# Kernel optimization log

Measured on AMD Instinct MI355X. Metric: run time of the kernel, lower is better.

Reference implementation:

```python
import jax, jax.numpy as jnp
import numpy as np

GAMMA = 1.0

def _rbf_mean(a, b, gamma):
    # mean of exp(-gamma * ||a_i - b_j||^2) over the full [Na, Nb] kernel matrix
    aa = jnp.sum(a * a, axis=1, keepdims=True)          # [Na, 1]
    bb = jnp.sum(b * b, axis=1, keepdims=True)          # [Nb, 1]
    dist = aa + bb.T - 2.0 * (a @ b.T)                  # [Na, Nb]
    return jnp.mean(jnp.exp(-gamma * dist))

def setup_inputs() -> dict:
    key = jax.random.key(0)
    kx, ky = jax.random.split(key)
    N, D = 8192, 128
    x = jax.random.normal(kx, (N, D), dtype=jnp.float32)
    y = jax.random.normal(ky, (N, D), dtype=jnp.float32)
    return {"x": x, "y": y}

def reference(x, y):
    mmd = (_rbf_mean(x, x, GAMMA)
           + _rbf_mean(y, y, GAMMA)
           - 2.0 * _rbf_mean(x, y, GAMMA))
    return mmd
```

## Files before the change

kernel.cpp:

```cpp
#include <hip/hip_runtime.h>


#define N_PTS 8192
#define DCOLS 128
#define TILE 128
#define TJ 64
#define NSELF 2080
#define NJOBS 8256
#define NBLOCKS 768
#define LOG2E 1.4426950408889634f
#define THRESH -40.0f
#define QS 24.0f
#define INV_S2 (1.0f / (QS * QS))

typedef __attribute__((ext_vector_type(4))) int int4v;
typedef unsigned int u32;
typedef unsigned short u16;
typedef unsigned char u8;

#if __has_builtin(__builtin_amdgcn_exp2f)
#define EXP2(x) __builtin_amdgcn_exp2f(x)
#else
#define EXP2(x) exp2f(x)
#endif

__device__ __forceinline__ int vmax(int a, int b) { return a > b ? a : b; }

__device__ __forceinline__ void gl_lds16(const u8* g, u8* l) {
  __builtin_amdgcn_global_load_lds(
      (const __attribute__((address_space(1))) u32*)g,
      (__attribute__((address_space(3))) u32*)l, 16, 0, 0);
}

__global__ void prep_kernel(const float* __restrict__ x, const float* __restrict__ y,
                            u32* __restrict__ xb, u32* __restrict__ yb,
                            float* __restrict__ da, float* __restrict__ db,
                            u32* __restrict__ Sz) {
  if (blockIdx.x == 0 && threadIdx.x < 4) Sz[threadIdx.x] = 0;
  int gt = blockIdx.x * 256 + threadIdx.x;
  int r = gt >> 5;
  int l31 = threadIdx.x & 31;
  const float* src;
  u32* dst;
  float* dn;
  int rr = r;
  if (r < N_PTS) { src = x; dst = xb; dn = da; }
  else           { src = y; dst = yb; dn = db; rr = r - N_PTS; }
  float4 v = ((const float4*)(src + (size_t)rr * 128))[l31];
  int q0 = (int)rintf(fminf(fmaxf(v.x * QS, -127.f), 127.f));
  int q1 = (int)rintf(fminf(fmaxf(v.y * QS, -127.f), 127.f));
  int q2 = (int)rintf(fminf(fmaxf(v.z * QS, -127.f), 127.f));
  int q3 = (int)rintf(fminf(fmaxf(v.w * QS, -127.f), 127.f));
  dst[(size_t)rr * 32 + l31] = (u32)(q0 & 0xff) | ((u32)(q1 & 0xff) << 8) |
                               ((u32)(q2 & 0xff) << 16) | ((u32)(q3 & 0xff) << 24);
  int p = q0 * q0 + q1 * q1 + q2 * q2 + q3 * q3;
#pragma unroll
  for (int off = 16; off; off >>= 1) p += __shfl_xor(p, off, 64);
  if (l31 == 0) dn[rr] = -LOG2E * INV_S2 * (float)p;
}

struct Job { int pair, rr, cc; };

__device__ __forceinline__ Job decode_job(int t) {
  Job jb;
  if (t < 2 * NSELF) {
    jb.pair = (t < NSELF) ? 0 : 1;
    int tt = t - jb.pair * NSELF;
    int r = 0;
    while (tt >= TJ - r) { tt -= TJ - r; r++; }
    jb.rr = r; jb.cc = r + tt;
  } else {
    int q = t - 2 * NSELF;
    jb.pair = 2; jb.rr = q >> 6; jb.cc = q & 63;
  }
  return jb;
}

__device__ __forceinline__ Job next_job(Job c) {
  Job n = c;
  if (c.pair == 2) {
    if (c.cc == 63) { n.rr++; n.cc = 0; } else n.cc++;
  } else {
    if (c.cc == 63) {
      if (c.rr == 63) { n.pair++; n.rr = 0; n.cc = 0; }
      else { n.rr++; n.cc = n.rr; }
    } else n.cc++;
  }
  return n;
}

__device__ __forceinline__ void pair_ptrs(int pair, const u8* xb, const u8* yb,
                                          const float* da, const float* db,
                                          const u8*& A, const u8*& B,
                                          const float*& dA, const float*& dB) {
  A = (pair == 1) ? yb : xb;
  B = (pair == 0) ? xb : yb;
  dA = (pair == 1) ? db : da;
  dB = (pair == 0) ? da : db;
}

__device__ __forceinline__ void stage_tile(const u8* gsrc, u8* ldst,
                                           int wid, int lane) {
  int r8 = lane >> 3, c7 = lane & 7;
  const u8* gl = gsrc + r8 * DCOLS + ((c7 ^ r8) << 4);
#pragma unroll
  for (int i = 0; i < 4; i++) {
    int blk = wid * 4 + i;
    gl_lds16(gl + blk * 1024, ldst + blk * 1024);
  }
}

__device__ __forceinline__ void load_astrip(const u8* gA, const float* gdA, int rr,
                                            int mbase, int quad, int l15,
                                            int4v afr[2][4], float& dmaxA) {
  const u8* base = gA + (size_t)rr * (TILE * DCOLS);
#pragma unroll
  for (int ks = 0; ks < 2; ks++)
#pragma unroll
    for (int mi = 0; mi < 4; mi++)
      afr[ks][mi] = *(const int4v*)(base + (mbase + mi * 16 + l15) * DCOLS +
                                    ks * 64 + quad * 16);
  const float* dr = gdA + rr * TILE + mbase;
  float m = dr[quad * 4];
#pragma unroll
  for (int mi = 0; mi < 4; mi++)
#pragma unroll
    for (int v = 0; v < 4; v++) m = fmaxf(m, dr[mi * 16 + quad * 4 + v]);
  dmaxA = m;
}

__global__ __launch_bounds__(256, 3) void mmd_kernel(
    const u8* __restrict__ xb, const u8* __restrict__ yb,
    const float* __restrict__ da, const float* __restrict__ db,
    float* __restrict__ S, u32* __restrict__ cnt, float* __restrict__ out) {
  __shared__ __align__(16) u8 Bt[2][TILE * DCOLS];

  int tid = threadIdx.x;
  int wid = tid >> 6, lane = tid & 63;
  int quad = lane >> 4, l15 = lane & 15;
  int mbase = (wid >> 1) * 64, nbase = (wid & 1) * 64;

  int start = (int)(((u32)blockIdx.x * NJOBS) / NBLOCKS);
  int end = (int)(((u32)(blockIdx.x + 1) * NJOBS) / NBLOCKS);

  Job cur = decode_job(start);
  const u8 *cA, *cB;
  const float *cdA, *cdB;
  pair_ptrs(cur.pair, xb, yb, da, db, cA, cB, cdA, cdB);

  int4v afr[2][4];
  float dmaxA;
  load_astrip(cA, cdA, cur.rr, mbase, quad, l15, afr, dmaxA);
  stage_tile(cB + (size_t)cur.cc * (TILE * DCOLS), &Bt[0][0], wid, lane);
  __syncthreads();

  const float c1 = 2.0f * LOG2E * INV_S2;
  float tsum = 0.f;
  int p = 0;

  for (int j = start; j < end; j++) {
    bool hasNext = (j + 1 < end);
    Job nxt;
    const u8 *nA = cA, *nB = cB;
    const float *ndA = cdA, *ndB = cdB;

    float dbn[4];
    {
      const float* dr = cdB + cur.cc * TILE + nbase;
#pragma unroll
      for (int ni = 0; ni < 4; ni++) dbn[ni] = dr[ni * 16 + l15];
    }

    if (hasNext) {
      nxt = next_job(cur);
      pair_ptrs(nxt.pair, xb, yb, da, db, nA, nB, ndA, ndB);
      stage_tile(nB + (size_t)nxt.cc * (TILE * DCOLS), &Bt[p ^ 1][0], wid, lane);
    }

    int4v acc[4][4];
    int4v zero = {0, 0, 0, 0};
#pragma unroll
    for (int mi = 0; mi < 4; mi++)
#pragma unroll
      for (int ni = 0; ni < 4; ni++) acc[mi][ni] = zero;

#pragma unroll
    for (int ks = 0; ks < 2; ks++) {
      int4v bf[4];
      int slot = ((ks * 4 + quad) ^ (l15 & 7)) << 4;
#pragma unroll
      for (int ni = 0; ni < 4; ni++) {
        int row = nbase + ni * 16 + l15;
        bf[ni] = *(const int4v*)(&Bt[p][row * DCOLS + slot]);
      }
#pragma unroll
      for (int mi = 0; mi < 4; mi++)
#pragma unroll
        for (int ni = 0; ni < 4; ni++)
          acc[mi][ni] = __builtin_amdgcn_mfma_i32_16x16x64_i8(
              afr[ks][mi], bf[ni], acc[mi][ni], 0, 0, 0);
    }

    int4v vm = acc[0][0];
#pragma unroll
    for (int mi = 0; mi < 4; mi++)
#pragma unroll
      for (int ni = 0; ni < 4; ni++) {
        if (mi == 0 && ni == 0) continue;
        int4v a = acc[mi][ni];
        vm[0] = vmax(vm[0], a[0]); vm[1] = vmax(vm[1], a[1]);
        vm[2] = vmax(vm[2], a[2]); vm[3] = vmax(vm[3], a[3]);
      }
    int imax = vmax(vmax(vm[0], vm[1]), vmax(vm[2], vm[3]));
    float dbmax = fmaxf(fmaxf(dbn[0], dbn[1]), fmaxf(dbn[2], dbn[3]));
    float bound = fmaf(c1, (float)imax, dmaxA + dbmax);

    if (__any(bound > THRESH)) {
      float w = (cur.pair < 2 && cur.rr != cur.cc) ? 2.0f : 1.0f;
      const float* dAex = cdA + cur.rr * TILE + mbase + quad * 4;
#pragma unroll
      for (int mi = 0; mi < 4; mi++) {
        const float* dv = dAex + mi * 16;
#pragma unroll
        for (int ni = 0; ni < 4; ni++) {
          int4v a = acc[mi][ni];
          float tv0 = fmaf(c1, (float)a[0], dv[0]);
          float tv1 = fmaf(c1, (float)a[1], dv[1]);
          float tv2 = fmaf(c1, (float)a[2], dv[2]);
          float tv3 = fmaf(c1, (float)a[3], dv[3]);
          float e = EXP2(tv0 + dbn[ni]) + EXP2(tv1 + dbn[ni]) +
                    EXP2(tv2 + dbn[ni]) + EXP2(tv3 + dbn[ni]);
          tsum = fmaf(w, e, tsum);
        }
      }
    }

    bool flush = !hasNext || (nxt.pair != cur.pair);
    if (flush) {
      float r = tsum;
#pragma unroll
      for (int off = 32; off; off >>= 1) r += __shfl_down(r, off, 64);
      if (lane == 0) atomicAdd(&S[cur.pair], r);
      tsum = 0.f;
    }

    if (hasNext && (nxt.pair != cur.pair || nxt.rr != cur.rr))
      load_astrip(nA, ndA, nxt.rr, mbase, quad, l15, afr, dmaxA);

    __syncthreads();
    p ^= 1;
    if (hasNext) { cur = nxt; cA = nA; cB = nB; cdA = ndA; cdB = ndB; }
  }

  __syncthreads();
  if (tid == 0) {
    __threadfence();
    u32 old = atomicAdd(cnt, 1u);
    if (old == (u32)(NBLOCKS - 1)) {
      float s0 = atomicAdd(&S[0], 0.0f);
      float s1 = atomicAdd(&S[1], 0.0f);
      float s2 = atomicAdd(&S[2], 0.0f);
      out[0] = (s0 + s1 - 2.0f * s2) * (1.0f / ((float)N_PTS * (float)N_PTS));
    }
  }
}

extern "C" void kernel_launch(void* const* d_in, const int* in_sizes, int n_in,
                              void* d_out, int out_size, void* d_ws, size_t ws_size,
                              hipStream_t stream) {
  const float* x = (const float*)d_in[0];
  const float* y = (const float*)d_in[1];
  char* ws = (char*)d_ws;
  float* S = (float*)ws;
  u32* cnt = (u32*)ws + 3;
  u8* xb = (u8*)(ws + 256);
  u8* yb = (u8*)(ws + 256 + (1 << 20));
  float* da = (float*)(ws + 256 + (2 << 20));
  float* db = (float*)(ws + 256 + (2 << 20) + 32768);

  prep_kernel<<<2048, 256, 0, stream>>>(x, y, (u32*)xb, (u32*)yb, da, db, (u32*)ws);
  mmd_kernel<<<NBLOCKS, 256, 0, stream>>>(xb, yb, da, db, S, cnt, (float*)d_out);
}
```

Before: 124.8 us.

## Process two B tiles per barrier step with four-slot LDS buffering

Restructures the main loop so each iteration handles two consecutive jobs, staging the next two B tiles into a second pair of LDS buffers while the current pair is computed. This halves the number of __syncthreads barriers per job and gives the async loads more time to land. LDS use doubles to 64KB per block, so occupancy drops to 2 blocks per CU, and the grid is cut from 768 to 512 blocks to match. Register pressure and control flow grow, and with fewer resident waves there is less latency hiding.

Result: faster. 110.5 us (-11.5%).

```diff
diff --git a/kernel.cpp b/kernel.cpp
--- a/kernel.cpp
+++ b/kernel.cpp
@@ -7,7 +7,7 @@
 #define TJ 64
 #define NSELF 2080
 #define NJOBS 8256
-#define NBLOCKS 768
+#define NBLOCKS 512
 #define LOG2E 1.4426950408889634f
 #define THRESH -40.0f
 #define QS 24.0f
@@ -89,14 +89,17 @@
   return n;
 }
 
-__device__ __forceinline__ void pair_ptrs(int pair, const u8* xb, const u8* yb,
-                                          const float* da, const float* db,
-                                          const u8*& A, const u8*& B,
-                                          const float*& dA, const float*& dB) {
-  A = (pair == 1) ? yb : xb;
-  B = (pair == 0) ? xb : yb;
-  dA = (pair == 1) ? db : da;
-  dB = (pair == 0) ? da : db;
+__device__ __forceinline__ const u8* Aptr(int pair, const u8* xb, const u8* yb) {
+  return (pair == 1) ? yb : xb;
+}
+__device__ __forceinline__ const u8* Bptr(int pair, const u8* xb, const u8* yb) {
+  return (pair == 0) ? xb : yb;
+}
+__device__ __forceinline__ const float* dAptr(int pair, const float* da, const float* db) {
+  return (pair == 1) ? db : da;
+}
+__device__ __forceinline__ const float* dBptr(int pair, const float* da, const float* db) {
+  return (pair == 0) ? da : db;
 }
 
 __device__ __forceinline__ void stage_tile(const u8* gsrc, u8* ldst,
@@ -129,11 +132,73 @@
   dmaxA = m;
 }
 
-__global__ __launch_bounds__(256, 3) void mmd_kernel(
+__device__ __forceinline__ void compute_tile(
+    const u8* __restrict__ Bs, const int4v afr[2][4], float dmaxA,
+    const float dbn[4], float w, const float* __restrict__ dAex,
+    float& tsum, int quad, int l15, float c1) {
+  int4v acc[4][4];
+  int4v zero = {0, 0, 0, 0};
+#pragma unroll
+  for (int mi = 0; mi < 4; mi++)
+#pragma unroll
+    for (int ni = 0; ni < 4; ni++) acc[mi][ni] = zero;
+
+  int nbase_l = 0;
+#pragma unroll
+  for (int ks = 0; ks < 2; ks++) {
+    int4v bf[4];
+    int slot = ((ks * 4 + quad) ^ (l15 & 7)) << 4;
+#pragma unroll
+    for (int ni = 0; ni < 4; ni++) {
+      int row = nbase_l + ni * 16 + l15;
+      bf[ni] = *(const int4v*)(&Bs[row * DCOLS + slot]);
+    }
+#pragma unroll
+    for (int mi = 0; mi < 4; mi++)
+#pragma unroll
+      for (int ni = 0; ni < 4; ni++)
+        acc[mi][ni] = __builtin_amdgcn_mfma_i32_16x16x64_i8(
+            afr[ks][mi], bf[ni], acc[mi][ni], 0, 0, 0);
+  }
+
+  int4v vm = acc[0][0];
+#pragma unroll
+  for (int mi = 0; mi < 4; mi++)
+#pragma unroll
+    for (int ni = 0; ni < 4; ni++) {
+      if (mi == 0 && ni == 0) continue;
+      int4v a = acc[mi][ni];
+      vm[0] = vmax(vm[0], a[0]); vm[1] = vmax(vm[1], a[1]);
+      vm[2] = vmax(vm[2], a[2]); vm[3] = vmax(vm[3], a[3]);
+    }
+  int imax = vmax(vmax(vm[0], vm[1]), vmax(vm[2], vm[3]));
+  float dbmax = fmaxf(fmaxf(dbn[0], dbn[1]), fmaxf(dbn[2], dbn[3]));
+  float bound = fmaf(c1, (float)imax, dmaxA + dbmax);
+
+  if (__any(bound > THRESH)) {
+#pragma unroll
+    for (int mi = 0; mi < 4; mi++) {
+      const float* dv = dAex + mi * 16;
+#pragma unroll
+      for (int ni = 0; ni < 4; ni++) {
+        int4v a = acc[mi][ni];
+        float tv0 = fmaf(c1, (float)a[0], dv[0]);
+        float tv1 = fmaf(c1, (float)a[1], dv[1]);
+        float tv2 = fmaf(c1, (float)a[2], dv[2]);
+        float tv3 = fmaf(c1, (float)a[3], dv[3]);
+        float e = EXP2(tv0 + dbn[ni]) + EXP2(tv1 + dbn[ni]) +
+                  EXP2(tv2 + dbn[ni]) + EXP2(tv3 + dbn[ni]);
+        tsum = fmaf(w, e, tsum);
+      }
+    }
+  }
+}
+
+__global__ __launch_bounds__(256, 2) void mmd_kernel(
     const u8* __restrict__ xb, const u8* __restrict__ yb,
     const float* __restrict__ da, const float* __restrict__ db,
     float* __restrict__ S, u32* __restrict__ cnt, float* __restrict__ out) {
-  __shared__ __align__(16) u8 Bt[2][TILE * DCOLS];
+  __shared__ __align__(16) u8 Bt[2][2][TILE * DCOLS];
 
   int tid = threadIdx.x;
   int wid = tid >> 6, lane = tid & 63;
@@ -142,114 +207,100 @@
 
   int start = (int)(((u32)blockIdx.x * NJOBS) / NBLOCKS);
   int end = (int)(((u32)(blockIdx.x + 1) * NJOBS) / NBLOCKS);
-
-  Job cur = decode_job(start);
-  const u8 *cA, *cB;
-  const float *cdA, *cdB;
-  pair_ptrs(cur.pair, xb, yb, da, db, cA, cB, cdA, cdB);
+  int rem = end - start;
+
+  const float c1 = 2.0f * LOG2E * INV_S2;
+  float tsum = 0.f;
+
+  Job a = decode_job(start), b;
+  bool hasB = rem > 1;
+  if (hasB) b = next_job(a);
 
   int4v afr[2][4];
   float dmaxA;
-  load_astrip(cA, cdA, cur.rr, mbase, quad, l15, afr, dmaxA);
-  stage_tile(cB + (size_t)cur.cc * (TILE * DCOLS), &Bt[0][0], wid, lane);
+  int loadedPair = a.pair, loadedRr = a.rr;
+  load_astrip(Aptr(a.pair, xb, yb), dAptr(a.pair, da, db), a.rr,
+              mbase, quad, l15, afr, dmaxA);
+
+  stage_tile(Bptr(a.pair, xb, yb) + (size_t)a.cc * (TILE * DCOLS),
+             &Bt[0][0][0], wid, lane);
+  if (hasB)
+    stage_tile(Bptr(b.pair, xb, yb) + (size_t)b.cc * (TILE * DCOLS),
+               &Bt[0][1][0], wid, lane);
   __syncthreads();
 
-  const float c1 = 2.0f * LOG2E * INV_S2;
-  float tsum = 0.f;
   int p = 0;
-
-  for (int j = start; j < end; j++) {
-    bool hasNext = (j + 1 < end);
-    Job nxt;
-    const u8 *nA = cA, *nB = cB;
-    const float *ndA = cdA, *ndB = cdB;
-
-    float dbn[4];
+  while (rem > 0) {
+    int n = (rem > 1) ? 2 : 1;
+    int nrem = rem - n;
+    Job c, d;
+    bool hasC = nrem > 0, hasD = nrem > 1;
+    if (hasC) c = next_job(n == 2 ? b : a);
+    if (hasD) d = next_job(c);
+
+    float dbn0[4], dbn1[4];
     {
-      const float* dr = cdB + cur.cc * TILE + nbase;
-#pragma unroll
-      for (int ni = 0; ni < 4; ni++) dbn[ni] = dr[ni * 16 + l15];
-    }
-
-    if (hasNext) {
-      nxt = next_job(cur);
-      pair_ptrs(nxt.pair, xb, yb, da, db, nA, nB, ndA, ndB);
-      stage_tile(nB + (size_t)nxt.cc * (TILE * DCOLS), &Bt[p ^ 1][0], wid, lane);
-    }
-
-    int4v acc[4][4];
-    int4v zero = {0, 0, 0, 0};
-#pragma unroll
-    for (int mi = 0; mi < 4; mi++)
-#pragma unroll
-      for (int ni = 0; ni < 4; ni++) acc[mi][ni] = zero;
-
-#pragma unroll
-    for (int ks = 0; ks < 2; ks++) {
-      int4v bf[4];
-      int slot = ((ks * 4 + quad) ^ (l15 & 7)) << 4;
-#pragma unroll
-      for (int ni = 0; ni < 4; ni++) {
-        int row = nbase + ni * 16 + l15;
-        bf[ni] = *(const int4v*)(&Bt[p][row * DCOLS + slot]);
+      const float* dr = dBptr(a.pair, da, db) + a.cc * TILE + nbase;
+#pragma unroll
+      for (int ni = 0; ni < 4; ni++) dbn0[ni] = dr[ni * 16 + l15];
+    }
+    if (n == 2) {
+      const float* dr = dBptr(b.pair, da, db) + b.cc * TILE + nbase;
+#pragma unroll
+      for (int ni = 0; ni < 4; ni++) dbn1[ni] = dr[ni * 16 + l15];
+    }
+
+    if (hasC)
+      stage_tile(Bptr(c.pair, xb, yb) + (size_t)c.cc * (TILE * DCOLS),
+                 &Bt[p ^ 1][0][0], wid, lane);
+    if (hasD)
+      stage_tile(Bptr(d.pair, xb, yb) + (size_t)d.cc * (TILE * DCOLS),
+                 &Bt[p ^ 1][1][0], wid, lane);
+
+    {
+      float w = (a.pair < 2 && a.rr != a.cc) ? 2.0f : 1.0f;
+      const float* dAex = dAptr(a.pair, da, db) + a.rr * TILE + mbase + quad * 4;
+      compute_tile(&Bt[p][0][nbase * DCOLS], afr, dmaxA, dbn0, w, dAex,
+                   tsum, quad, l15, c1);
+      bool haveNextJob = (n == 2) || hasC;
+      int nextPair = (n == 2) ? b.pair : (hasC ? c.pair : -1);
+      if (!haveNextJob || nextPair != a.pair) {
+        float r = tsum;
+#pragma unroll
+        for (int off = 32; off; off >>= 1) r += __shfl_down(r, off, 64);
+        if (lane == 0) atomicAdd(&S[a.pair], r);
+        tsum = 0.f;
       }
-#pragma unroll
-      for (int mi = 0; mi < 4; mi++)
-#pragma unroll
-        for (int ni = 0; ni < 4; ni++)
-          acc[mi][ni] = __builtin_amdgcn_mfma_i32_16x16x64_i8(
-              afr[ks][mi], bf[ni], acc[mi][ni], 0, 0, 0);
-    }
-
-    int4v vm = acc[0][0];
-#pragma unroll
-    for (int mi = 0; mi < 4; mi++)
-#pragma unroll
-      for (int ni = 0; ni < 4; ni++) {
-        if (mi == 0 && ni == 0) continue;
-        int4v a = acc[mi][ni];
-        vm[0] = vmax(vm[0], a[0]); vm[1] = vmax(vm[1], a[1]);
-        vm[2] = vmax(vm[2], a[2]); vm[3] = vmax(vm[3], a[3]);
+    }
+
+    if (n == 2) {
+      if (b.pair != loadedPair || b.rr != loadedRr) {
+        loadedPair = b.pair; loadedRr = b.rr;
+        load_astrip(Aptr(b.pair, xb, yb), dAptr(b.pair, da, db), b.rr,
+                    mbase, quad, l15, afr, dmaxA);
       }
-    int imax = vmax(vmax(vm[0], vm[1]), vmax(vm[2], vm[3]));
-    float dbmax = fmaxf(fmaxf(dbn[0], dbn[1]), fmaxf(dbn[2], dbn[3]));
-    float bound = fmaf(c1, (float)imax, dmaxA + dbmax);
-
-    if (__any(bound > THRESH)) {
-      float w = (cur.pair < 2 && cur.rr != cur.cc) ? 2.0f : 1.0f;
-      const float* dAex = cdA + cur.rr * TILE + mbase + quad * 4;
-#pragma unroll
-      for (int mi = 0; mi < 4; mi++) {
-        const float* dv = dAex + mi * 16;
-#pragma unroll
-        for (int ni = 0; ni < 4; ni++) {
-          int4v a = acc[mi][ni];
-          float tv0 = fmaf(c1, (float)a[0], dv[0]);
-          float tv1 = fmaf(c1, (float)a[1], dv[1]);
-          float tv2 = fmaf(c1, (float)a[2], dv[2]);
-          float tv3 = fmaf(c1, (float)a[3], dv[3]);
-          float e = EXP2(tv0 + dbn[ni]) + EXP2(tv1 + dbn[ni]) +
-                    EXP2(tv2 + dbn[ni]) + EXP2(tv3 + dbn[ni]);
-          tsum = fmaf(w, e, tsum);
-        }
+      float w = (b.pair < 2 && b.rr != b.cc) ? 2.0f : 1.0f;
+      const float* dAex = dAptr(b.pair, da, db) + b.rr * TILE + mbase + quad * 4;
+      compute_tile(&Bt[p][1][nbase * DCOLS], afr, dmaxA, dbn1, w, dAex,
+                   tsum, quad, l15, c1);
+      if (!hasC || c.pair != b.pair) {
+        float r = tsum;
+#pragma unroll
+        for (int off = 32; off; off >>= 1) r += __shfl_down(r, off, 64);
+        if (lane == 0) atomicAdd(&S[b.pair], r);
+        tsum = 0.f;
       }
     }
 
-    bool flush = !hasNext || (nxt.pair != cur.pair);
-    if (flush) {
-      float r = tsum;
-#pragma unroll
-      for (int off = 32; off; off >>= 1) r += __shfl_down(r, off, 64);
-      if (lane == 0) atomicAdd(&S[cur.pair], r);
-      tsum = 0.f;
-    }
-
-    if (hasNext && (nxt.pair != cur.pair || nxt.rr != cur.rr))
-      load_astrip(nA, ndA, nxt.rr, mbase, quad, l15, afr, dmaxA);
+    if (hasC && (c.pair != loadedPair || c.rr != loadedRr)) {
+      loadedPair = c.pair; loadedRr = c.rr;
+      load_astrip(Aptr(c.pair, xb, yb), dAptr(c.pair, da, db), c.rr,
+                  mbase, quad, l15, afr, dmaxA);
+    }
 
     __syncthreads();
     p ^= 1;
-    if (hasNext) { cur = nxt; cA = nA; cB = nB; cdA = ndA; cdB = ndB; }
+    a = c; b = d; rem = nrem;
   }
 
   __syncthreads();
```
